# Performance work log

Measured on AMD Instinct MI355X. Metric: run time of the kernel, lower is better.

## Reference

```python
import jax, jax.numpy as jnp
import numpy as np

B, N, D, K = 4, 4096, 128, 20

def setup_inputs() -> dict:
    key = jax.random.key(0)
    k1, k2, k3 = jax.random.split(key, 3)
    s = 1.0 / np.sqrt(D)
    return {
        "x": jax.random.normal(k1, (B, N, D), dtype=jnp.float32),
        "Wq": jax.random.normal(k2, (D, D), dtype=jnp.float32) * s,
        "bq": jnp.zeros((D,), dtype=jnp.float32),
        "Wk": jax.random.normal(k3, (D, D), dtype=jnp.float32) * s,
        "bk": jnp.zeros((D,), dtype=jnp.float32),
    }

def reference(x, Wq, bq, Wk, bk):
    # Q/K projections: [B,N,D]
    Q = jnp.einsum('bnd,de->bne', x, Wq) + bq
    Kp = jnp.einsum('bnd,de->bne', x, Wk) + bk
    # scores: [B,N,N], scaled by sqrt(D)
    attn = jnp.einsum('bnd,bmd->bnm', Q, Kp) / jnp.sqrt(jnp.float32(D))
    # top-k along last dim -> binary mask via scatter
    _, topk_idx = jax.lax.top_k(attn, K)  # [B,N,K]
    bi = jnp.arange(B)[:, None, None]
    ni = jnp.arange(N)[None, :, None]
    mask = jnp.zeros_like(attn).at[bi, ni, topk_idx].set(1.0)
    # zero out non-topk entries, then full softmax over all N (zeros included,
    # matching the torch module exactly)
    sparse_attn = attn * mask
    out = jax.nn.softmax(sparse_attn, axis=-1)
    return out[..., None]  # [B,N,N,1]
```

## Files before the change

kernel.cpp:

```cpp
#include <hip/hip_runtime.h>

#define BN 4096
#define BD 128
#define NB 4
#define TOPK 20
#define CAND 128
#define EPS 0.06f

typedef float f32x4 __attribute__((ext_vector_type(4)));
typedef short bf16x8 __attribute__((ext_vector_type(8)));

__device__ inline unsigned short f2bf(float f) {
  unsigned int u = __float_as_uint(f);
  unsigned int r = (u + 0x7FFFu + ((u >> 16) & 1u)) >> 16;
  return (unsigned short)r;
}

__global__ __launch_bounds__(256) void proj_kernel(
    const float* __restrict__ x,
    const float* __restrict__ Wq, const float* __restrict__ bq,
    const float* __restrict__ Wk, const float* __restrict__ bk,
    double* __restrict__ Qd, double* __restrict__ Kd, unsigned short* __restrict__ Khi) {
  __shared__ double xs[32][129];
  const int tid = threadIdx.x;
  const long row0 = (long)blockIdx.x * 32;
  const float* xsrc = x + row0 * BD;
  for (int i = tid; i < 32 * BD; i += 256) xs[i >> 7][i & 127] = (double)xsrc[i];
  __syncthreads();

  const int e = tid & 127;
  const bool isK = tid >= 128;
  const float* W = isK ? Wk : Wq;
  const float* bias = isK ? bk : bq;
  double* Od = isK ? Kd : Qd;

  double acc[32];
  const double binit = (double)bias[e];
#pragma unroll
  for (int r = 0; r < 32; ++r) acc[r] = binit;

  for (int d = 0; d < BD; ++d) {
    const double wv = (double)W[d * BD + e];
#pragma unroll
    for (int r = 0; r < 32; ++r) acc[r] = fma(xs[r][d], wv, acc[r]);
  }

#pragma unroll
  for (int r = 0; r < 32; ++r) {
    const double a = acc[r];
    const long o = (row0 + r) * BD + e;
    Od[o] = a;
    if (isK) Khi[o] = f2bf((float)a);
  }
}

__global__ __launch_bounds__(512) void screen_kernel(
    const double* __restrict__ Qd, const unsigned short* __restrict__ Khi,
    unsigned short* __restrict__ cand, unsigned int* __restrict__ cnt) {
  const int tid = threadIdx.x;
  const int lane = tid & 63;
  const int w = tid >> 6;
  const int blk = blockIdx.x;
  const int b = (blk & 7) >> 1;
  const int i = ((blk >> 3) << 1) | (blk & 1);
  const int rowbase = i << 5;
  const int lq = lane & 15;
  const int gg = lane >> 4;
  const float RS = 0.088388347648318447f;

  __shared__ float pool[32][64];
  __shared__ float tauLds[32];
  __shared__ unsigned int scnt[32];
  __shared__ unsigned short slist[32][CAND];

  bf16x8 bqf[2][4];
#pragma unroll
  for (int t2 = 0; t2 < 2; ++t2) {
    const double* qp = Qd + ((long)b * BN + rowbase + t2 * 16 + lq) * BD;
#pragma unroll
    for (int ks = 0; ks < 4; ++ks) {
      const int dbase = ks * 32 + gg * 8;
      bf16x8 pk;
#pragma unroll
      for (int j = 0; j < 8; ++j) pk[j] = (short)f2bf((float)qp[dbase + j]);
      bqf[t2][ks] = pk;
    }
  }

  const unsigned short* kb = Khi + (long)b * BN * BD;
  const long arow = (long)lq * BD + gg * 8;
  const int t0 = w * 32;
  const unsigned short* tb0 = kb + (long)t0 * 16 * BD + arow;

  float t1a = -3.4e38f, t2a = -3.4e38f, t1b = -3.4e38f, t2b = -3.4e38f;
  bf16x8 a[4], an[4];
#pragma unroll
  for (int ks = 0; ks < 4; ++ks) a[ks] = *(const bf16x8*)(tb0 + ks * 32);
  for (int tt = 0; tt < 32; ++tt) {
    if (tt < 31) {
      const unsigned short* nb = kb + (long)(t0 + tt + 1) * 16 * BD + arow;
#pragma unroll
      for (int ks = 0; ks < 4; ++ks) an[ks] = *(const bf16x8*)(nb + ks * 32);
    }
    f32x4 acc0 = {0.f, 0.f, 0.f, 0.f}, acc1 = {0.f, 0.f, 0.f, 0.f};
#pragma unroll
    for (int ks = 0; ks < 4; ++ks) {
      acc0 = __builtin_amdgcn_mfma_f32_16x16x32_bf16(a[ks], bqf[0][ks], acc0, 0, 0, 0);
      acc1 = __builtin_amdgcn_mfma_f32_16x16x32_bf16(a[ks], bqf[1][ks], acc1, 0, 0, 0);
    }
#pragma unroll
    for (int reg = 0; reg < 4; ++reg) {
      const float s0 = acc0[reg] * RS;
      const float m1a = fmaxf(t1a, s0);
      t2a = fmaxf(t2a, fminf(t1a, s0));
      t1a = m1a;
      const float s1 = acc1[reg] * RS;
      const float m1b = fmaxf(t1b, s1);
      t2b = fmaxf(t2b, fminf(t1b, s1));
      t1b = m1b;
    }
#pragma unroll
    for (int ks = 0; ks < 4; ++ks) a[ks] = an[ks];
  }

  pool[lq][w * 8 + gg * 2 + 0] = t1a;
  pool[lq][w * 8 + gg * 2 + 1] = t2a;
  pool[16 + lq][w * 8 + gg * 2 + 0] = t1b;
  pool[16 + lq][w * 8 + gg * 2 + 1] = t2b;
  if (tid < 32) scnt[tid] = 0;
  __syncthreads();

  for (int rr = 0; rr < 4; ++rr) {
    const int r = w * 4 + rr;
    float v = pool[r][lane];
#pragma unroll
    for (int k = 2; k <= 64; k <<= 1) {
#pragma unroll
      for (int j = k >> 1; j > 0; j >>= 1) {
        const float o = __shfl_xor(v, j);
        const bool keepmin = (((lane & k) == 0) == ((lane & j) == 0));
        v = keepmin ? fminf(v, o) : fmaxf(v, o);
      }
    }
    const float tau = __shfl(v, 44);
    if (lane == 0) tauLds[r] = tau;
  }
  __syncthreads();

  const float tha = tauLds[lq] - EPS;
  const float thb = tauLds[16 + lq] - EPS;

#pragma unroll
  for (int ks = 0; ks < 4; ++ks) a[ks] = *(const bf16x8*)(tb0 + ks * 32);
  for (int tt = 0; tt < 32; ++tt) {
    if (tt < 31) {
      const unsigned short* nb = kb + (long)(t0 + tt + 1) * 16 * BD + arow;
#pragma unroll
      for (int ks = 0; ks < 4; ++ks) an[ks] = *(const bf16x8*)(nb + ks * 32);
    }
    f32x4 acc0 = {0.f, 0.f, 0.f, 0.f}, acc1 = {0.f, 0.f, 0.f, 0.f};
#pragma unroll
    for (int ks = 0; ks < 4; ++ks) {
      acc0 = __builtin_amdgcn_mfma_f32_16x16x32_bf16(a[ks], bqf[0][ks], acc0, 0, 0, 0);
      acc1 = __builtin_amdgcn_mfma_f32_16x16x32_bf16(a[ks], bqf[1][ks], acc1, 0, 0, 0);
    }
#pragma unroll
    for (int reg = 0; reg < 4; ++reg) {
      const int col = (t0 + tt) * 16 + gg * 4 + reg;
      const float s0 = acc0[reg] * RS;
      if (s0 >= tha) {
        unsigned int p = atomicAdd(&scnt[lq], 1u);
        if (p < CAND) slist[lq][p] = (unsigned short)col;
      }
      const float s1 = acc1[reg] * RS;
      if (s1 >= thb) {
        unsigned int p = atomicAdd(&scnt[16 + lq], 1u);
        if (p < CAND) slist[16 + lq][p] = (unsigned short)col;
      }
    }
#pragma unroll
    for (int ks = 0; ks < 4; ++ks) a[ks] = an[ks];
  }
  __syncthreads();

  const long growbase = (long)b * BN + rowbase;
  if (tid < 32) cnt[growbase + tid] = min(scnt[tid], (unsigned int)CAND);
  const unsigned short* sl = &slist[0][0];
  for (int j = tid; j < 32 * CAND; j += 512) cand[growbase * CAND + j] = sl[j];
}

__device__ inline float rescore_f64(const double2* __restrict__ kp2, const double2* __restrict__ q2) {
  double a0 = 0.0, a1 = 0.0, a2 = 0.0, a3 = 0.0;
#pragma unroll
  for (int i = 0; i < 64; i += 4) {
    a0 = fma(q2[i + 0].y, kp2[i + 0].y, fma(q2[i + 0].x, kp2[i + 0].x, a0));
    a1 = fma(q2[i + 1].y, kp2[i + 1].y, fma(q2[i + 1].x, kp2[i + 1].x, a1));
    a2 = fma(q2[i + 2].y, kp2[i + 2].y, fma(q2[i + 2].x, kp2[i + 2].x, a2));
    a3 = fma(q2[i + 3].y, kp2[i + 3].y, fma(q2[i + 3].x, kp2[i + 3].x, a3));
  }
  return (float)(((a0 + a1) + (a2 + a3)) * 8.8388347648318447e-02);
}

__global__ __launch_bounds__(512) void finalize_kernel(
    const double* __restrict__ Qd, const double* __restrict__ Kd,
    const unsigned short* __restrict__ cand, const unsigned int* __restrict__ cnt,
    float* __restrict__ out) {
  __shared__ double qsd[16][BD];
  __shared__ float lutval[16][TOPK];
  __shared__ int lutcol[16][TOPK];
  __shared__ float rowc0[16];

  const int tid = threadIdx.x;
  const int lane = tid & 63;
  const int w = tid >> 6;
  const int blk = blockIdx.x;
  const int b = blk >> 8;
  const int row0 = (blk & 255) << 4;

  {
    const double* qsrc = Qd + ((long)b * BN + row0) * BD;
    double* qdst = &qsd[0][0];
    for (int i = tid; i < 16 * BD; i += 512) qdst[i] = qsrc[i];
  }
  __syncthreads();

  float* outrow = out + ((long)b * BN + row0) * BN;
  const double* kb = Kd + (long)b * BN * BD;

  for (int rr = 0; rr < 2; ++rr) {
    const int r = w + rr * 8;
    const long grow = (long)b * BN + row0 + r;
    const int c = (int)min(cnt[grow], (unsigned int)CAND);

    int kv0 = 0x7fffffff, kv1 = 0x7fffffff;
    float v0 = -3.4e38f, v1 = -3.4e38f;
    if (lane < c) {
      kv0 = (int)cand[grow * CAND + lane];
      v0 = rescore_f64((const double2*)(kb + (long)kv0 * BD), (const double2*)&qsd[r][0]);
    }
    if (lane + 64 < c) {
      kv1 = (int)cand[grow * CAND + lane + 64];
      v1 = rescore_f64((const double2*)(kb + (long)kv1 * BD), (const double2*)&qsd[r][0]);
    }
    if (v1 > v0 || (v1 == v0 && kv1 < kv0)) {
      float tv = v0; v0 = v1; v1 = tv;
      int tk = kv0; kv0 = kv1; kv1 = tk;
    }

    float m = 0.0f, se = 0.0f;
    for (int it = 0; it < TOPK; ++it) {
      float rv = v0;
      int rc = kv0;
      for (int off = 32; off; off >>= 1) {
        const float ov = __shfl_xor(rv, off);
        const int oc = __shfl_xor(rc, off);
        if (ov > rv || (ov == rv && oc < rc)) { rv = ov; rc = oc; }
      }
      if (it == 0) m = fmaxf(rv, 0.0f);
      se += expf(rv - m);
      if (lane == 0) { lutval[r][it] = rv; lutcol[r][it] = rc; }
      if (kv0 == rc) { v0 = v1; kv0 = kv1; v1 = -3.4e38f; kv1 = 0x7fffffff; }
    }

    const float Z = se + (float)(BN - TOPK) * expf(-m);
    if (lane < TOPK) lutval[r][lane] = expf(lutval[r][lane] - m) / Z;
    if (lane == 0) rowc0[r] = expf(-m) / Z;
  }
  __syncthreads();

  for (int r = 0; r < 16; ++r) {
    const float c0 = rowc0[r];
    const float4 cv = make_float4(c0, c0, c0, c0);
    float4* op = ((float4*)(outrow + (long)r * BN)) + w * 128 + lane * 2;
    op[0] = cv;
    op[1] = cv;
  }
  __syncthreads();

  if (tid < 16 * TOPK) {
    const int r = tid / TOPK;
    const int k = tid % TOPK;
    outrow[(long)r * BN + lutcol[r][k]] = lutval[r][k];
  }
}

extern "C" void kernel_launch(void* const* d_in, const int* in_sizes, int n_in,
                              void* d_out, int out_size, void* d_ws, size_t ws_size,
                              hipStream_t stream) {
  const float* x  = (const float*)d_in[0];
  const float* Wq = (const float*)d_in[1];
  const float* bq = (const float*)d_in[2];
  const float* Wk = (const float*)d_in[3];
  const float* bk = (const float*)d_in[4];
  float* out = (float*)d_out;

  const long NE = (long)NB * BN * BD;
  double* Qd = (double*)d_ws;
  double* Kd = Qd + NE;
  unsigned short* Khi = (unsigned short*)(Kd + NE);
  unsigned short* cand = Khi + NE;
  unsigned int* cnt = (unsigned int*)(cand + (long)NB * BN * CAND);

  proj_kernel<<<NB * BN / 32, 256, 0, stream>>>(x, Wq, bq, Wk, bk, Qd, Kd, Khi);
  screen_kernel<<<NB * (BN / 32), 512, 0, stream>>>(Qd, Khi, cand, cnt);
  finalize_kernel<<<NB * (BN / 16), 512, 0, stream>>>(Qd, Kd, cand, cnt, out);
}
```

Before: 321.8 us.

## Halve screen rows per block and run finalize as one row per wave

```diff
diff --git a/kernel.cpp b/kernel.cpp
--- a/kernel.cpp
+++ b/kernel.cpp
@@ -63,75 +63,63 @@
   const int blk = blockIdx.x;
   const int b = (blk & 7) >> 1;
   const int i = ((blk >> 3) << 1) | (blk & 1);
-  const int rowbase = i << 5;
+  const int rowbase = i << 4;
   const int lq = lane & 15;
   const int gg = lane >> 4;
   const float RS = 0.088388347648318447f;
 
-  __shared__ float pool[32][64];
-  __shared__ float tauLds[32];
-  __shared__ unsigned int scnt[32];
-  __shared__ unsigned short slist[32][CAND];
-
-  bf16x8 bqf[2][4];
-#pragma unroll
-  for (int t2 = 0; t2 < 2; ++t2) {
-    const double* qp = Qd + ((long)b * BN + rowbase + t2 * 16 + lq) * BD;
+  __shared__ float pool[16][64];
+  __shared__ float tauLds[16];
+  __shared__ unsigned int scnt[16];
+  __shared__ unsigned short slist[16][CAND];
+
+  if (tid < 16) scnt[tid] = 0;
+
+  bf16x8 bqf[4];
+  {
+    const double* qp = Qd + ((long)b * BN + rowbase + lq) * BD;
 #pragma unroll
     for (int ks = 0; ks < 4; ++ks) {
       const int dbase = ks * 32 + gg * 8;
       bf16x8 pk;
 #pragma unroll
       for (int j = 0; j < 8; ++j) pk[j] = (short)f2bf((float)qp[dbase + j]);
-      bqf[t2][ks] = pk;
+      bqf[ks] = pk;
     }
   }
 
   const unsigned short* kb = Khi + (long)b * BN * BD;
   const long arow = (long)lq * BD + gg * 8;
   const int t0 = w * 32;
-  const unsigned short* tb0 = kb + (long)t0 * 16 * BD + arow;
-
-  float t1a = -3.4e38f, t2a = -3.4e38f, t1b = -3.4e38f, t2b = -3.4e38f;
-  bf16x8 a[4], an[4];
-#pragma unroll
-  for (int ks = 0; ks < 4; ++ks) a[ks] = *(const bf16x8*)(tb0 + ks * 32);
+
+  float t1 = -3.4e38f, t2 = -3.4e38f;
+  bf16x8 a[4];
+#pragma unroll
+  for (int ks = 0; ks < 4; ++ks)
+    a[ks] = *(const bf16x8*)(kb + (long)t0 * 16 * BD + arow + ks * 32);
   for (int tt = 0; tt < 32; ++tt) {
-    if (tt < 31) {
-      const unsigned short* nb = kb + (long)(t0 + tt + 1) * 16 * BD + arow;
-#pragma unroll
-      for (int ks = 0; ks < 4; ++ks) an[ks] = *(const bf16x8*)(nb + ks * 32);
-    }
-    f32x4 acc0 = {0.f, 0.f, 0.f, 0.f}, acc1 = {0.f, 0.f, 0.f, 0.f};
+    const unsigned short* nb = kb + (long)(t0 + tt + 1) * 16 * BD + arow;
+    f32x4 acc = {0.f, 0.f, 0.f, 0.f};
 #pragma unroll
     for (int ks = 0; ks < 4; ++ks) {
-      acc0 = __builtin_amdgcn_mfma_f32_16x16x32_bf16(a[ks], bqf[0][ks], acc0, 0, 0, 0);
-      acc1 = __builtin_amdgcn_mfma_f32_16x16x32_bf16(a[ks], bqf[1][ks], acc1, 0, 0, 0);
+      acc = __builtin_amdgcn_mfma_f32_16x16x32_bf16(a[ks], bqf[ks], acc, 0, 0, 0);
+      a[ks] = *(const bf16x8*)(nb + ks * 32);
     }
 #pragma unroll
     for (int reg = 0; reg < 4; ++reg) {
-      const float s0 = acc0[reg] * RS;
-      const float m1a = fmaxf(t1a, s0);
-      t2a = fmaxf(t2a, fminf(t1a, s0));
-      t1a = m1a;
-      const float s1 = acc1[reg] * RS;
-      const float m1b = fmaxf(t1b, s1);
-      t2b = fmaxf(t2b, fminf(t1b, s1));
-      t1b = m1b;
-    }
-#pragma unroll
-    for (int ks = 0; ks < 4; ++ks) a[ks] = an[ks];
-  }
-
-  pool[lq][w * 8 + gg * 2 + 0] = t1a;
-  pool[lq][w * 8 + gg * 2 + 1] = t2a;
-  pool[16 + lq][w * 8 + gg * 2 + 0] = t1b;
-  pool[16 + lq][w * 8 + gg * 2 + 1] = t2b;
-  if (tid < 32) scnt[tid] = 0;
-  __syncthreads();
-
-  for (int rr = 0; rr < 4; ++rr) {
-    const int r = w * 4 + rr;
+      const float s = acc[reg] * RS;
+      const float m1 = fmaxf(t1, s);
+      t2 = fmaxf(t2, fminf(t1, s));
+      t1 = m1;
+    }
+  }
+
+  pool[lq][w * 8 + gg * 2 + 0] = t1;
+  pool[lq][w * 8 + gg * 2 + 1] = t2;
+  __syncthreads();
+
+  for (int rr = 0; rr < 2; ++rr) {
+    const int r = w * 2 + rr;
     float v = pool[r][lane];
 #pragma unroll
     for (int k = 2; k <= 64; k <<= 1) {
@@ -147,46 +135,34 @@
   }
   __syncthreads();
 
-  const float tha = tauLds[lq] - EPS;
-  const float thb = tauLds[16 + lq] - EPS;
-
-#pragma unroll
-  for (int ks = 0; ks < 4; ++ks) a[ks] = *(const bf16x8*)(tb0 + ks * 32);
+  const float th = tauLds[lq] - EPS;
+
+#pragma unroll
+  for (int ks = 0; ks < 4; ++ks)
+    a[ks] = *(const bf16x8*)(kb + (long)t0 * 16 * BD + arow + ks * 32);
   for (int tt = 0; tt < 32; ++tt) {
-    if (tt < 31) {
-      const unsigned short* nb = kb + (long)(t0 + tt + 1) * 16 * BD + arow;
-#pragma unroll
-      for (int ks = 0; ks < 4; ++ks) an[ks] = *(const bf16x8*)(nb + ks * 32);
-    }
-    f32x4 acc0 = {0.f, 0.f, 0.f, 0.f}, acc1 = {0.f, 0.f, 0.f, 0.f};
+    const unsigned short* nb = kb + (long)(t0 + tt + 1) * 16 * BD + arow;
+    f32x4 acc = {0.f, 0.f, 0.f, 0.f};
 #pragma unroll
     for (int ks = 0; ks < 4; ++ks) {
-      acc0 = __builtin_amdgcn_mfma_f32_16x16x32_bf16(a[ks], bqf[0][ks], acc0, 0, 0, 0);
-      acc1 = __builtin_amdgcn_mfma_f32_16x16x32_bf16(a[ks], bqf[1][ks], acc1, 0, 0, 0);
+      acc = __builtin_amdgcn_mfma_f32_16x16x32_bf16(a[ks], bqf[ks], acc, 0, 0, 0);
+      a[ks] = *(const bf16x8*)(nb + ks * 32);
     }
 #pragma unroll
     for (int reg = 0; reg < 4; ++reg) {
-      const int col = (t0 + tt) * 16 + gg * 4 + reg;
-      const float s0 = acc0[reg] * RS;
-      if (s0 >= tha) {
+      const float s = acc[reg] * RS;
+      if (s >= th) {
         unsigned int p = atomicAdd(&scnt[lq], 1u);
-        if (p < CAND) slist[lq][p] = (unsigned short)col;
+        if (p < CAND) slist[lq][p] = (unsigned short)((t0 + tt) * 16 + gg * 4 + reg);
       }
-      const float s1 = acc1[reg] * RS;
-      if (s1 >= thb) {
-        unsigned int p = atomicAdd(&scnt[16 + lq], 1u);
-        if (p < CAND) slist[16 + lq][p] = (unsigned short)col;
-      }
-    }
-#pragma unroll
-    for (int ks = 0; ks < 4; ++ks) a[ks] = an[ks];
+    }
   }
   __syncthreads();
 
   const long growbase = (long)b * BN + rowbase;
-  if (tid < 32) cnt[growbase + tid] = min(scnt[tid], (unsigned int)CAND);
+  if (tid < 16) cnt[growbase + tid] = min(scnt[tid], (unsigned int)CAND);
   const unsigned short* sl = &slist[0][0];
-  for (int j = tid; j < 32 * CAND; j += 512) cand[growbase * CAND + j] = sl[j];
+  for (int j = tid; j < 16 * CAND; j += 512) cand[growbase * CAND + j] = sl[j];
 }
 
 __device__ inline float rescore_f64(const double2* __restrict__ kp2, const double2* __restrict__ q2) {
@@ -201,87 +177,69 @@
   return (float)(((a0 + a1) + (a2 + a3)) * 8.8388347648318447e-02);
 }
 
-__global__ __launch_bounds__(512) void finalize_kernel(
+__device__ inline unsigned int fmono(float v) {
+  const unsigned int u = __float_as_uint(v);
+  return (u & 0x80000000u) ? ~u : (u | 0x80000000u);
+}
+__device__ inline float fdemono(unsigned int k) {
+  const unsigned int u = (k & 0x80000000u) ? (k & 0x7fffffffu) : ~k;
+  return __uint_as_float(u);
+}
+
+__global__ __launch_bounds__(256) void finalize_kernel(
     const double* __restrict__ Qd, const double* __restrict__ Kd,
     const unsigned short* __restrict__ cand, const unsigned int* __restrict__ cnt,
     float* __restrict__ out) {
-  __shared__ double qsd[16][BD];
-  __shared__ float lutval[16][TOPK];
-  __shared__ int lutcol[16][TOPK];
-  __shared__ float rowc0[16];
-
   const int tid = threadIdx.x;
   const int lane = tid & 63;
   const int w = tid >> 6;
-  const int blk = blockIdx.x;
-  const int b = blk >> 8;
-  const int row0 = (blk & 255) << 4;
-
-  {
-    const double* qsrc = Qd + ((long)b * BN + row0) * BD;
-    double* qdst = &qsd[0][0];
-    for (int i = tid; i < 16 * BD; i += 512) qdst[i] = qsrc[i];
-  }
-  __syncthreads();
-
-  float* outrow = out + ((long)b * BN + row0) * BN;
+  const long row = (long)blockIdx.x * 4 + w;
+  const int b = (int)(row >> 12);
+  float* outrow = out + row * BN;
   const double* kb = Kd + (long)b * BN * BD;
-
-  for (int rr = 0; rr < 2; ++rr) {
-    const int r = w + rr * 8;
-    const long grow = (long)b * BN + row0 + r;
-    const int c = (int)min(cnt[grow], (unsigned int)CAND);
-
-    int kv0 = 0x7fffffff, kv1 = 0x7fffffff;
-    float v0 = -3.4e38f, v1 = -3.4e38f;
-    if (lane < c) {
-      kv0 = (int)cand[grow * CAND + lane];
-      v0 = rescore_f64((const double2*)(kb + (long)kv0 * BD), (const double2*)&qsd[r][0]);
-    }
-    if (lane + 64 < c) {
-      kv1 = (int)cand[grow * CAND + lane + 64];
-      v1 = rescore_f64((const double2*)(kb + (long)kv1 * BD), (const double2*)&qsd[r][0]);
-    }
-    if (v1 > v0 || (v1 == v0 && kv1 < kv0)) {
-      float tv = v0; v0 = v1; v1 = tv;
-      int tk = kv0; kv0 = kv1; kv1 = tk;
-    }
-
-    float m = 0.0f, se = 0.0f;
-    for (int it = 0; it < TOPK; ++it) {
-      float rv = v0;
-      int rc = kv0;
-      for (int off = 32; off; off >>= 1) {
-        const float ov = __shfl_xor(rv, off);
-        const int oc = __shfl_xor(rc, off);
-        if (ov > rv || (ov == rv && oc < rc)) { rv = ov; rc = oc; }
-      }
-      if (it == 0) m = fmaxf(rv, 0.0f);
-      se += expf(rv - m);
-      if (lane == 0) { lutval[r][it] = rv; lutcol[r][it] = rc; }
-      if (kv0 == rc) { v0 = v1; kv0 = kv1; v1 = -3.4e38f; kv1 = 0x7fffffff; }
-    }
-
-    const float Z = se + (float)(BN - TOPK) * expf(-m);
-    if (lane < TOPK) lutval[r][lane] = expf(lutval[r][lane] - m) / Z;
-    if (lane == 0) rowc0[r] = expf(-m) / Z;
-  }
-  __syncthreads();
-
-  for (int r = 0; r < 16; ++r) {
-    const float c0 = rowc0[r];
-    const float4 cv = make_float4(c0, c0, c0, c0);
-    float4* op = ((float4*)(outrow + (long)r * BN)) + w * 128 + lane * 2;
-    op[0] = cv;
-    op[1] = cv;
-  }
-  __syncthreads();
-
-  if (tid < 16 * TOPK) {
-    const int r = tid / TOPK;
-    const int k = tid % TOPK;
-    outrow[(long)r * BN + lutcol[r][k]] = lutval[r][k];
-  }
+  const double2* q2 = (const double2*)(Qd + row * BD);
+
+  const int c = (int)min(cnt[row], (unsigned int)CAND);
+
+  unsigned long long key0 = 0ull, key1 = 0ull;
+  if (lane < c) {
+    const int kv = (int)cand[row * CAND + lane];
+    const float v = rescore_f64((const double2*)(kb + (long)kv * BD), q2);
+    key0 = ((unsigned long long)fmono(v) << 12) | (unsigned int)(4095 - kv);
+  }
+  if (lane + 64 < c) {
+    const int kv = (int)cand[row * CAND + lane + 64];
+    const float v = rescore_f64((const double2*)(kb + (long)kv * BD), q2);
+    key1 = ((unsigned long long)fmono(v) << 12) | (unsigned int)(4095 - kv);
+  }
+  if (key1 > key0) { const unsigned long long t = key0; key0 = key1; key1 = t; }
+
+  float m = 0.0f, se = 0.0f;
+  float myval = 0.0f;
+  int mycol = 0;
+  for (int it = 0; it < TOPK; ++it) {
+    unsigned long long rk = key0;
+    for (int off = 32; off; off >>= 1) {
+      const unsigned long long ok = __shfl_xor(rk, off);
+      rk = (ok > rk) ? ok : rk;
+    }
+    const float rv = fdemono((unsigned int)(rk >> 12));
+    if (it == 0) m = fmaxf(rv, 0.0f);
+    se += expf(rv - m);
+    if (lane == it) { myval = rv; mycol = 4095 - (int)(rk & 0xFFFull); }
+    if (key0 == rk) { key0 = key1; key1 = 0ull; }
+  }
+
+  const float Z = se + (float)(BN - TOPK) * expf(-m);
+  const float c0 = expf(-m) / Z;
+
+  const float4 cv = make_float4(c0, c0, c0, c0);
+  float4* op = (float4*)outrow;
+#pragma unroll
+  for (int i = 0; i < 16; ++i) op[i * 64 + lane] = cv;
+
+  asm volatile("s_waitcnt vmcnt(0)" ::: "memory");
+  if (lane < TOPK) outrow[mycol] = expf(myval - m) / Z;
 }
 
 extern "C" void kernel_launch(void* const* d_in, const int* in_sizes, int n_in,
@@ -302,6 +260,6 @@
   unsigned int* cnt = (unsigned int*)(cand + (long)NB * BN * CAND);
 
   proj_kernel<<<NB * BN / 32, 256, 0, stream>>>(x, Wq, bq, Wk, bk, Qd, Kd, Khi);
-  screen_kernel<<<NB * (BN / 32), 512, 0, stream>>>(Qd, Khi, cand, cnt);
-  finalize_kernel<<<NB * (BN / 16), 512, 0, stream>>>(Qd, Kd, cand, cnt, out);
-}
+  screen_kernel<<<NB * (BN / 16), 512, 0, stream>>>(Qd, Khi, cand, cnt);
+  finalize_kernel<<<NB * BN / 4, 256, 0, stream>>>(Qd, Kd, cand, cnt, out);
+}
```

New measurement: 434.9 us. 1.35x slower.
